# Kernel tuning notes

Measured on AMD Instinct MI355X. Metric: run time of the kernel, lower is better.

The kernel has to match this reference:

```python
import jax, jax.numpy as jnp
jax.config.update("jax_enable_x64", True)
import numpy as np


def _quat_to_rot(q):
    q = q / jnp.linalg.norm(q)
    a, b, c, d = q[0], q[1], q[2], q[3]
    return jnp.stack([
        1 - 2 * c * c - 2 * d * d, 2 * b * c - 2 * a * d, 2 * a * c + 2 * b * d,
        2 * b * c + 2 * a * d, 1 - 2 * b * b - 2 * d * d, 2 * c * d - 2 * a * b,
        2 * b * d - 2 * a * c, 2 * a * b + 2 * c * d, 1 - 2 * b * b - 2 * c * c,
    ]).reshape(3, 3)


def _chamfer(x, y):
    # x: [N,4], y: [M,4]; fp64 cdist + bidirectional min-reduction (memory-bound)
    x = x.astype(jnp.float64)
    y = y.astype(jnp.float64)
    d2 = (jnp.sum(x * x, -1)[:, None] + jnp.sum(y * y, -1)[None, :]
          - 2.0 * x @ y.T)
    d = jnp.sqrt(jnp.maximum(d2, 0.0))
    return jnp.min(d, axis=1).mean() + jnp.min(d, axis=0).mean()


def _revolute_transform(anchor, axis, theta):
    # anchor: [3] (a,b,c), axis: [3] (u,v,w), theta scalar -> 4x4 screw rotation
    a, b, c = anchor[0], anchor[1], anchor[2]
    u, v, w = axis[0], axis[1], axis[2]
    cos = jnp.cos(theta)
    sin = jnp.sin(theta)
    top = jnp.stack([
        u * u + (v * v + w * w) * cos, u * v * (1 - cos) - w * sin, u * w * (1 - cos) + v * sin,
        (a * (v * v + w * w) - u * (b * v + c * w)) * (1 - cos) + (b * w - c * v) * sin,
        u * v * (1 - cos) + w * sin, v * v + (u * u + w * w) * cos, v * w * (1 - cos) - u * sin,
        (b * (u * u + w * w) - v * (a * u + c * w)) * (1 - cos) + (c * u - a * w) * sin,
        u * w * (1 - cos) - v * sin, v * w * (1 - cos) + u * sin, w * w + (u * u + v * v) * cos,
        (c * (u * u + v * v) - w * (a * u + b * v)) * (1 - cos) + (a * v - b * u) * sin,
    ]).reshape(3, 4)
    bottom = jnp.array([[0.0, 0.0, 0.0, 1.0]], dtype=top.dtype)
    return jnp.concatenate([top, bottom], axis=0)


def setup_inputs() -> dict:
    key = jax.random.key(0)
    ks = jax.random.split(key, 8)
    P, N = 2, 8192
    return {
        "camera_pts": jax.random.normal(ks[0], (P, N, 3), dtype=jnp.float32),
        "cad_pts": jax.random.normal(ks[1], (P, N, 3), dtype=jnp.float32),
        "xyz": jax.random.normal(ks[2], (P - 1, 3), dtype=jnp.float32),
        "rpy": jax.random.normal(ks[3], (P - 1, 3), dtype=jnp.float32),
        "part_weight": jax.random.uniform(ks[4], (P,), dtype=jnp.float32),
        "base_r_quat": jax.random.normal(ks[5], (4,), dtype=jnp.float32),
        "base_t": jax.random.normal(ks[6], (3, 1), dtype=jnp.float32),
        "joint_state": jax.random.normal(ks[7], (P - 1,), dtype=jnp.float32),
    }


def reference(camera_pts, cad_pts, xyz, rpy, part_weight, base_r_quat, base_t, joint_state):
    num_parts = camera_pts.shape[0]
    num_joints = num_parts - 1
    ones = jnp.ones(camera_pts.shape[:-1] + (1,), dtype=camera_pts.dtype)
    cam_h = jnp.concatenate([camera_pts, ones], axis=-1)  # [P,N,4]
    cad_h = jnp.concatenate([cad_pts, ones], axis=-1)     # [P,N,4]

    base_rot = _quat_to_rot(base_r_quat)
    base_transform = jnp.concatenate([
        jnp.concatenate([base_rot, base_t], axis=1),
        jnp.array([[0.0, 0.0, 0.0, 1.0]], dtype=base_rot.dtype),
    ], axis=0)  # 4x4

    cad_base = cad_h[0] @ base_transform.T
    base_objective = _chamfer(cad_base, cam_h[0])
    all_objective = part_weight[0] * base_objective

    child_objectives = []
    rel_transforms = []
    for j in range(num_joints):
        rel = _revolute_transform(xyz[j], rpy[j], joint_state[j])
        rel_transforms.append(rel)
        T = rel @ base_transform
        cad_child = cad_h[j + 1] @ T.T
        obj = _chamfer(cad_child, cam_h[j + 1])
        child_objectives.append(obj)
        all_objective = all_objective + part_weight[j + 1] * obj

    all_objective = all_objective / num_parts
    relative_transform_all = jnp.stack(rel_transforms, axis=0)
    child_objective_all = jnp.stack(child_objectives, axis=0)
    return (all_objective, base_objective, child_objective_all,
            base_transform, relative_transform_all)
```

## Files before the change

### kernel.cpp

```cpp
#include <hip/hip_runtime.h>
#include <math.h>

#define NPTS 8192

struct Xforms { float B[3][4]; float R[3][4]; float T[3][4]; };

__device__ __forceinline__ void compute_xforms(const float* __restrict__ quat,
                                               const float* __restrict__ bt,
                                               const float* __restrict__ anchor,
                                               const float* __restrict__ axis,
                                               const float* __restrict__ theta,
                                               Xforms& X) {
  float q0 = quat[0], q1 = quat[1], q2 = quat[2], q3 = quat[3];
  float n = sqrtf(q0 * q0 + q1 * q1 + q2 * q2 + q3 * q3);
  float a = q0 / n, b = q1 / n, c = q2 / n, d = q3 / n;
  X.B[0][0] = 1.f - 2.f * c * c - 2.f * d * d;
  X.B[0][1] = 2.f * b * c - 2.f * a * d;
  X.B[0][2] = 2.f * a * c + 2.f * b * d;
  X.B[0][3] = bt[0];
  X.B[1][0] = 2.f * b * c + 2.f * a * d;
  X.B[1][1] = 1.f - 2.f * b * b - 2.f * d * d;
  X.B[1][2] = 2.f * c * d - 2.f * a * b;
  X.B[1][3] = bt[1];
  X.B[2][0] = 2.f * b * d - 2.f * a * c;
  X.B[2][1] = 2.f * a * b + 2.f * c * d;
  X.B[2][2] = 1.f - 2.f * b * b - 2.f * c * c;
  X.B[2][3] = bt[2];

  float ax = anchor[0], ay = anchor[1], az = anchor[2];
  float u = axis[0], v = axis[1], w = axis[2];
  float th = theta[0];
  float cs = cosf(th), sn = sinf(th), oc = 1.f - cs;
  X.R[0][0] = u * u + (v * v + w * w) * cs;
  X.R[0][1] = u * v * oc - w * sn;
  X.R[0][2] = u * w * oc + v * sn;
  X.R[0][3] = (ax * (v * v + w * w) - u * (ay * v + az * w)) * oc + (ay * w - az * v) * sn;
  X.R[1][0] = u * v * oc + w * sn;
  X.R[1][1] = v * v + (u * u + w * w) * cs;
  X.R[1][2] = v * w * oc - u * sn;
  X.R[1][3] = (ay * (u * u + w * w) - v * (ax * u + az * w)) * oc + (az * u - ax * w) * sn;
  X.R[2][0] = u * w * oc - v * sn;
  X.R[2][1] = v * w * oc + u * sn;
  X.R[2][2] = w * w + (u * u + v * v) * cs;
  X.R[2][3] = (az * (u * u + v * v) - w * (ax * u + ay * v)) * oc + (ax * v - ay * u) * sn;

#pragma unroll
  for (int i = 0; i < 3; i++) {
#pragma unroll
    for (int j = 0; j < 4; j++) {
      float s = X.R[i][0] * X.B[0][j] + X.R[i][1] * X.B[1][j] + X.R[i][2] * X.B[2][j];
      if (j == 3) s += X.R[i][3];
      X.T[i][j] = s;
    }
  }
}

__global__ __launch_bounds__(256) void prep_kernel(
    const float* __restrict__ cam, const float* __restrict__ cad,
    const float* __restrict__ quat, const float* __restrict__ bt,
    const float* __restrict__ anchor, const float* __restrict__ axis,
    const float* __restrict__ theta,
    float4* __restrict__ pts4, unsigned int* __restrict__ minarr,
    float* __restrict__ sums, unsigned int* __restrict__ counter) {
  int gid = blockIdx.x * 256 + threadIdx.x;
  minarr[gid] = 0x7f800000u;
  if (gid < 4) sums[gid] = 0.f;
  if (gid == 0) *counter = 0u;

  Xforms X;
  compute_xforms(quat, bt, anchor, axis, theta, X);

  int a = gid >> 13;
  int i = gid & 8191;
  int part = a >> 1;
  const float* base = ((a & 1) ? cam : cad) + part * NPTS * 3;
  float px = base[i * 3 + 0], py = base[i * 3 + 1], pz = base[i * 3 + 2];
  if ((a & 1) == 0) {
    float M[3][4];
#pragma unroll
    for (int r = 0; r < 3; r++)
#pragma unroll
      for (int cc = 0; cc < 4; cc++) M[r][cc] = part ? X.T[r][cc] : X.B[r][cc];
    float qx = M[0][0] * px + M[0][1] * py + M[0][2] * pz + M[0][3];
    float qy = M[1][0] * px + M[1][1] * py + M[1][2] * pz + M[1][3];
    float qz = M[2][0] * px + M[2][1] * py + M[2][2] * pz + M[2][3];
    px = qx; py = qy; pz = qz;
  }
  float h = 0.5f * (px * px + py * py + pz * pz);
  pts4[gid] = make_float4(px, py, pz, h);
}

__global__ __launch_bounds__(256) void chamfer_kernel(
    const float4* __restrict__ pts4, unsigned int* __restrict__ minarr) {
  const int combo = blockIdx.z;
  const int tid = threadIdx.x;
  const float4* __restrict__ srcp = pts4 + combo * NPTS;
  const float4* __restrict__ tgtp = pts4 + (combo ^ 1) * NPTS;

  const int sbase = blockIdx.x * 2048;

  float4 s[8];
  float vmin[8];
#pragma unroll
  for (int i = 0; i < 8; i++) {
    s[i] = srcp[sbase + i * 256 + tid];
    vmin[i] = 3.4e38f;
  }

  __shared__ float4 tile[256];
  tile[tid] = tgtp[blockIdx.y * 256 + tid];
  __syncthreads();

#pragma unroll 4
  for (int k = 0; k < 256; k++) {
    float4 t = tile[k];
#pragma unroll
    for (int i = 0; i < 8; i++) {
      float v = fmaf(-s[i].z, t.z, t.w);
      v = fmaf(-s[i].y, t.y, v);
      v = fmaf(-s[i].x, t.x, v);
      vmin[i] = fminf(vmin[i], v);
    }
  }

#pragma unroll
  for (int i = 0; i < 8; i++) {
    float d2 = fmaxf(0.f, 2.f * (s[i].w + vmin[i]));
    atomicMin(minarr + combo * NPTS + sbase + i * 256 + tid, __float_as_uint(d2));
  }
}

__global__ __launch_bounds__(256) void reduce_finalize_kernel(
    const unsigned int* __restrict__ minarr, float* __restrict__ sums,
    unsigned int* __restrict__ counter,
    const float* __restrict__ pw,
    const float* __restrict__ quat, const float* __restrict__ bt,
    const float* __restrict__ anchor, const float* __restrict__ axis,
    const float* __restrict__ theta, float* __restrict__ out) {
  const int tid = threadIdx.x;
  const int combo = blockIdx.x >> 3;
  const int chunk = blockIdx.x & 7;
  const int base = combo * NPTS + chunk * 1024;

  float ssum = 0.f;
#pragma unroll
  for (int j = 0; j < 4; j++)
    ssum += sqrtf(__uint_as_float(minarr[base + j * 256 + tid]));

#pragma unroll
  for (int off = 32; off > 0; off >>= 1) ssum += __shfl_down(ssum, off);
  __shared__ float part[4];
  if ((tid & 63) == 0) part[tid >> 6] = ssum;
  __syncthreads();

  if (tid == 0) {
    float blocksum = part[0] + part[1] + part[2] + part[3];
    atomicAdd(&sums[combo], blocksum);
    __threadfence();
    unsigned int old = atomicAdd(counter, 1u);
    if (old == 31u) {
      __threadfence();
      float s0 = __hip_atomic_load(&sums[0], __ATOMIC_ACQUIRE, __HIP_MEMORY_SCOPE_AGENT);
      float s1 = __hip_atomic_load(&sums[1], __ATOMIC_ACQUIRE, __HIP_MEMORY_SCOPE_AGENT);
      float s2 = __hip_atomic_load(&sums[2], __ATOMIC_ACQUIRE, __HIP_MEMORY_SCOPE_AGENT);
      float s3 = __hip_atomic_load(&sums[3], __ATOMIC_ACQUIRE, __HIP_MEMORY_SCOPE_AGENT);
      Xforms X;
      compute_xforms(quat, bt, anchor, axis, theta, X);
      const float inv = 1.0f / (float)NPTS;
      float base_obj = (s0 + s1) * inv;
      float child_obj = (s2 + s3) * inv;
      out[0] = (pw[0] * base_obj + pw[1] * child_obj) * 0.5f;
      out[1] = base_obj;
      out[2] = child_obj;
      for (int i = 0; i < 3; i++)
        for (int j = 0; j < 4; j++) out[3 + i * 4 + j] = X.B[i][j];
      out[15] = 0.f; out[16] = 0.f; out[17] = 0.f; out[18] = 1.f;
      for (int i = 0; i < 3; i++)
        for (int j = 0; j < 4; j++) out[19 + i * 4 + j] = X.R[i][j];
      out[31] = 0.f; out[32] = 0.f; out[33] = 0.f; out[34] = 1.f;
    }
  }
}

extern "C" void kernel_launch(void* const* d_in, const int* in_sizes, int n_in,
                              void* d_out, int out_size, void* d_ws, size_t ws_size,
                              hipStream_t stream) {
  const float* cam  = (const float*)d_in[0];
  const float* cad  = (const float*)d_in[1];
  const float* xyz  = (const float*)d_in[2];
  const float* rpy  = (const float*)d_in[3];
  const float* pw   = (const float*)d_in[4];
  const float* quat = (const float*)d_in[5];
  const float* bt   = (const float*)d_in[6];
  const float* js   = (const float*)d_in[7];

  unsigned int* minarr = (unsigned int*)d_ws;
  float4* pts4 = (float4*)((char*)d_ws + 4 * NPTS * sizeof(unsigned int));
  float* sums = (float*)((char*)d_ws + 4 * NPTS * sizeof(unsigned int) + 4 * NPTS * sizeof(float4));
  unsigned int* counter = (unsigned int*)(sums + 4);
  float* out = (float*)d_out;

  hipLaunchKernelGGL(prep_kernel, dim3(128), dim3(256), 0, stream,
                     cam, cad, quat, bt, xyz, rpy, js, pts4, minarr, sums, counter);
  hipLaunchKernelGGL(chamfer_kernel, dim3(4, 32, 4), dim3(256), 0, stream,
                     pts4, minarr);
  hipLaunchKernelGGL(reduce_finalize_kernel, dim3(32), dim3(256), 0, stream,
                     minarr, sums, counter, pw, quat, bt, xyz, rpy, js, out);
}
```

Baseline: 102.1 us.

## Fuse point transform into chamfer kernel and replace atomicMin with partial-min buffer

Removes the separate prep kernel by transforming raw xyz points inside the chamfer kernel, both for the source registers and the shared tile. Replaces per-point atomicMin into a global min array with plain stores into a per-chunk partial buffer, which the reduce kernel then min-reduces across 32 chunks. It also processes two tile entries per inner iteration. The goal is to save one kernel launch and avoid atomic contention. In exchange, every block recomputes the transforms, the reads are strided 3-float loads, and the reduce kernel has to read a 4 MB partial buffer.

```diff
diff --git a/kernel.cpp b/kernel.cpp
--- a/kernel.cpp
+++ b/kernel.cpp
@@ -2,6 +2,7 @@
 #include <math.h>
 
 #define NPTS 8192
+#define NCHUNK 32
 
 struct Xforms { float B[3][4]; float R[3][4]; float T[3][4]; };
 
@@ -55,83 +56,92 @@
   }
 }
 
-__global__ __launch_bounds__(256) void prep_kernel(
+__global__ __launch_bounds__(256) void chamfer_kernel(
     const float* __restrict__ cam, const float* __restrict__ cad,
     const float* __restrict__ quat, const float* __restrict__ bt,
     const float* __restrict__ anchor, const float* __restrict__ axis,
     const float* __restrict__ theta,
-    float4* __restrict__ pts4, unsigned int* __restrict__ minarr,
-    float* __restrict__ sums, unsigned int* __restrict__ counter) {
-  int gid = blockIdx.x * 256 + threadIdx.x;
-  minarr[gid] = 0x7f800000u;
-  if (gid < 4) sums[gid] = 0.f;
-  if (gid == 0) *counter = 0u;
+    float* __restrict__ partial, float* __restrict__ sums,
+    unsigned int* __restrict__ counter) {
+  const int combo = blockIdx.z;
+  const int tid = threadIdx.x;
+
+  if (blockIdx.x == 0 && blockIdx.y == 0 && combo == 0) {
+    if (tid < 4) sums[tid] = 0.f;
+    if (tid == 4) *counter = 0u;
+  }
 
   Xforms X;
   compute_xforms(quat, bt, anchor, axis, theta, X);
 
-  int a = gid >> 13;
-  int i = gid & 8191;
-  int part = a >> 1;
-  const float* base = ((a & 1) ? cam : cad) + part * NPTS * 3;
-  float px = base[i * 3 + 0], py = base[i * 3 + 1], pz = base[i * 3 + 2];
-  if ((a & 1) == 0) {
-    float M[3][4];
-#pragma unroll
-    for (int r = 0; r < 3; r++)
-#pragma unroll
-      for (int cc = 0; cc < 4; cc++) M[r][cc] = part ? X.T[r][cc] : X.B[r][cc];
-    float qx = M[0][0] * px + M[0][1] * py + M[0][2] * pz + M[0][3];
-    float qy = M[1][0] * px + M[1][1] * py + M[1][2] * pz + M[1][3];
-    float qz = M[2][0] * px + M[2][1] * py + M[2][2] * pz + M[2][3];
-    px = qx; py = qy; pz = qz;
-  }
-  float h = 0.5f * (px * px + py * py + pz * pz);
-  pts4[gid] = make_float4(px, py, pz, h);
-}
-
-__global__ __launch_bounds__(256) void chamfer_kernel(
-    const float4* __restrict__ pts4, unsigned int* __restrict__ minarr) {
-  const int combo = blockIdx.z;
-  const int tid = threadIdx.x;
-  const float4* __restrict__ srcp = pts4 + combo * NPTS;
-  const float4* __restrict__ tgtp = pts4 + (combo ^ 1) * NPTS;
+  const int part = combo >> 1;
+  const int src_is_cad = ((combo & 1) == 0) ? 1 : 0;
+
+  float Ms[3][4], Mt[3][4];
+#pragma unroll
+  for (int r = 0; r < 3; r++) {
+#pragma unroll
+    for (int c = 0; c < 4; c++) {
+      float m = part ? X.T[r][c] : X.B[r][c];
+      float id = (r == c) ? 1.f : 0.f;
+      Ms[r][c] = src_is_cad ? m : id;
+      Mt[r][c] = src_is_cad ? id : m;
+    }
+  }
+
+  const float* __restrict__ srcbase = (src_is_cad ? cad : cam) + part * NPTS * 3;
+  const float* __restrict__ tgtbase = (src_is_cad ? cam : cad) + part * NPTS * 3;
 
   const int sbase = blockIdx.x * 2048;
-
   float4 s[8];
   float vmin[8];
 #pragma unroll
   for (int i = 0; i < 8; i++) {
-    s[i] = srcp[sbase + i * 256 + tid];
+    int idx = (sbase + i * 256 + tid) * 3;
+    float px = srcbase[idx + 0], py = srcbase[idx + 1], pz = srcbase[idx + 2];
+    float qx = Ms[0][0] * px + Ms[0][1] * py + Ms[0][2] * pz + Ms[0][3];
+    float qy = Ms[1][0] * px + Ms[1][1] * py + Ms[1][2] * pz + Ms[1][3];
+    float qz = Ms[2][0] * px + Ms[2][1] * py + Ms[2][2] * pz + Ms[2][3];
+    s[i] = make_float4(qx, qy, qz, 0.5f * (qx * qx + qy * qy + qz * qz));
     vmin[i] = 3.4e38f;
   }
 
   __shared__ float4 tile[256];
-  tile[tid] = tgtp[blockIdx.y * 256 + tid];
+  {
+    int idx = (blockIdx.y * 256 + tid) * 3;
+    float px = tgtbase[idx + 0], py = tgtbase[idx + 1], pz = tgtbase[idx + 2];
+    float qx = Mt[0][0] * px + Mt[0][1] * py + Mt[0][2] * pz + Mt[0][3];
+    float qy = Mt[1][0] * px + Mt[1][1] * py + Mt[1][2] * pz + Mt[1][3];
+    float qz = Mt[2][0] * px + Mt[2][1] * py + Mt[2][2] * pz + Mt[2][3];
+    tile[tid] = make_float4(qx, qy, qz, 0.5f * (qx * qx + qy * qy + qz * qz));
+  }
   __syncthreads();
 
-#pragma unroll 4
-  for (int k = 0; k < 256; k++) {
-    float4 t = tile[k];
+#pragma unroll 2
+  for (int k = 0; k < 256; k += 2) {
+    float4 t0 = tile[k];
+    float4 t1 = tile[k + 1];
 #pragma unroll
     for (int i = 0; i < 8; i++) {
-      float v = fmaf(-s[i].z, t.z, t.w);
-      v = fmaf(-s[i].y, t.y, v);
-      v = fmaf(-s[i].x, t.x, v);
-      vmin[i] = fminf(vmin[i], v);
-    }
-  }
-
+      float v0 = fmaf(-s[i].z, t0.z, t0.w);
+      v0 = fmaf(-s[i].y, t0.y, v0);
+      v0 = fmaf(-s[i].x, t0.x, v0);
+      float v1 = fmaf(-s[i].z, t1.z, t1.w);
+      v1 = fmaf(-s[i].y, t1.y, v1);
+      v1 = fmaf(-s[i].x, t1.x, v1);
+      vmin[i] = fminf(vmin[i], fminf(v0, v1));
+    }
+  }
+
+  float* __restrict__ pp = partial + (combo * NCHUNK + blockIdx.y) * NPTS + sbase;
 #pragma unroll
   for (int i = 0; i < 8; i++) {
-    float d2 = fmaxf(0.f, 2.f * (s[i].w + vmin[i]));
-    atomicMin(minarr + combo * NPTS + sbase + i * 256 + tid, __float_as_uint(d2));
+    pp[i * 256 + tid] = fmaxf(0.f, 2.f * (s[i].w + vmin[i]));
   }
 }
 
 __global__ __launch_bounds__(256) void reduce_finalize_kernel(
-    const unsigned int* __restrict__ minarr, float* __restrict__ sums,
+    const float* __restrict__ partial, float* __restrict__ sums,
     unsigned int* __restrict__ counter,
     const float* __restrict__ pw,
     const float* __restrict__ quat, const float* __restrict__ bt,
@@ -140,12 +150,18 @@
   const int tid = threadIdx.x;
   const int combo = blockIdx.x >> 3;
   const int chunk = blockIdx.x & 7;
-  const int base = combo * NPTS + chunk * 1024;
-
-  float ssum = 0.f;
-#pragma unroll
-  for (int j = 0; j < 4; j++)
-    ssum += sqrtf(__uint_as_float(minarr[base + j * 256 + tid]));
+  const int sofs = chunk * 1024;
+
+  float m0 = 3.4e38f, m1 = 3.4e38f, m2 = 3.4e38f, m3 = 3.4e38f;
+#pragma unroll 8
+  for (int t = 0; t < NCHUNK; t++) {
+    const float* __restrict__ p = partial + (combo * NCHUNK + t) * NPTS + sofs;
+    m0 = fminf(m0, p[0 * 256 + tid]);
+    m1 = fminf(m1, p[1 * 256 + tid]);
+    m2 = fminf(m2, p[2 * 256 + tid]);
+    m3 = fminf(m3, p[3 * 256 + tid]);
+  }
+  float ssum = sqrtf(m0) + sqrtf(m1) + sqrtf(m2) + sqrtf(m3);
 
 #pragma unroll
   for (int off = 32; off > 0; off >>= 1) ssum += __shfl_down(ssum, off);
@@ -194,16 +210,13 @@
   const float* bt   = (const float*)d_in[6];
   const float* js   = (const float*)d_in[7];
 
-  unsigned int* minarr = (unsigned int*)d_ws;
-  float4* pts4 = (float4*)((char*)d_ws + 4 * NPTS * sizeof(unsigned int));
-  float* sums = (float*)((char*)d_ws + 4 * NPTS * sizeof(unsigned int) + 4 * NPTS * sizeof(float4));
+  float* partial = (float*)d_ws;
+  float* sums = (float*)((char*)d_ws + 4 * NCHUNK * NPTS * sizeof(float));
   unsigned int* counter = (unsigned int*)(sums + 4);
   float* out = (float*)d_out;
 
-  hipLaunchKernelGGL(prep_kernel, dim3(128), dim3(256), 0, stream,
-                     cam, cad, quat, bt, xyz, rpy, js, pts4, minarr, sums, counter);
-  hipLaunchKernelGGL(chamfer_kernel, dim3(4, 32, 4), dim3(256), 0, stream,
-                     pts4, minarr);
+  hipLaunchKernelGGL(chamfer_kernel, dim3(4, NCHUNK, 4), dim3(256), 0, stream,
+                     cam, cad, quat, bt, xyz, rpy, js, partial, sums, counter);
   hipLaunchKernelGGL(reduce_finalize_kernel, dim3(32), dim3(256), 0, stream,
-                     minarr, sums, counter, pw, quat, bt, xyz, rpy, js, out);
-}
+                     partial, sums, counter, pw, quat, bt, xyz, rpy, js, out);
+}
```

New measurement: 100.5 us. Within noise of the previous version (-1.5%).
